# Optimization experiments

Measured on AMD Instinct MI355X. Metric: run time of the kernel, lower is better.

The kernel has to match this reference:

```python
import jax, jax.numpy as jnp
import numpy as np

B, S, D = 4, 2048, 1024
H = 16
DK = D // H  # 64

def setup_inputs() -> dict:
    key = jax.random.key(0)
    ks = jax.random.split(key, 5)
    scale = 0.02
    return {
        "x": jax.random.normal(ks[0], (B, S, D), dtype=jnp.float32),
        "Wq": jax.random.normal(ks[1], (D, D), dtype=jnp.float32) * scale,
        "Wk": jax.random.normal(ks[2], (D, D), dtype=jnp.float32) * scale,
        "Wv": jax.random.normal(ks[3], (D, D), dtype=jnp.float32) * scale,
        "Wo": jax.random.normal(ks[4], (D, D), dtype=jnp.float32) * scale,
    }

def reference(x, Wq, Wk, Wv, Wo):
    b, s, d = x.shape
    h, dk = H, DK
    # torch nn.Linear(bias=False): y = x @ W.T
    q = (x @ Wq.T).reshape(b, s, h, dk).transpose(0, 2, 1, 3)  # [b,h,s,dk]
    k = (x @ Wk.T).reshape(b, s, h, dk).transpose(0, 2, 1, 3)
    v = (x @ Wv.T).reshape(b, s, h, dk).transpose(0, 2, 1, 3)
    scores = jnp.einsum('bhqd,bhkd->bhqk', q, k) * (dk ** -0.5)
    causal = jnp.triu(jnp.ones((s, s), dtype=bool), k=1)  # True = masked out
    scores = jnp.where(causal, -jnp.inf, scores)
    probs = jax.nn.softmax(scores, axis=-1)
    attn = jnp.einsum('bhqk,bhkd->bhqd', probs, v)  # [b,h,s,dk]
    attn = attn.transpose(0, 2, 1, 3).reshape(b, s, d)
    return attn @ Wo.T
```

## Files before the change

### kernel.cpp

```cpp
#include <hip/hip_runtime.h>

typedef __attribute__((ext_vector_type(8))) short bf16x8;
typedef __attribute__((ext_vector_type(4))) float f32x4;
typedef __attribute__((ext_vector_type(2))) unsigned int u32x2;
typedef unsigned int u32;
typedef unsigned short u16;

constexpr int Bb = 4, S = 2048, D = 1024, H = 16, DK = 64, M = Bb * S;

#if __has_builtin(__builtin_amdgcn_exp2f)
#define EXP2F __builtin_amdgcn_exp2f
#else
#define EXP2F exp2f
#endif

__device__ __forceinline__ u16 f2bf(float f) {
  u32 u = __float_as_uint(f);
  return (u16)((u + 0x7fffu + ((u >> 16) & 1u)) >> 16);
}

__device__ __forceinline__ u32 cvt_pk_bf16(float a, float b) {
  u32 r;
  asm("v_cvt_pk_bf16_f32 %0, %1, %2" : "=v"(r) : "v"(a), "v"(b));
  return r;
}

__device__ __forceinline__ void gld_lds16(const u16* g, u16* l) {
  __builtin_amdgcn_global_load_lds((const __attribute__((address_space(1))) u32*)g,
                                   (__attribute__((address_space(3))) u32*)l, 16, 0, 0);
}

struct CastAll { const float* s[5]; u16* d[5]; float sc[5]; };
__global__ __launch_bounds__(256) void cast_all_kernel(CastAll a) {
  int bid = blockIdx.x;
  int w, off;
  if (bid < 4096) { w = bid >> 10; off = ((bid & 1023) * 256 + threadIdx.x) * 4; }
  else            { w = 4;         off = ((bid - 4096) * 256 + threadIdx.x) * 4; }
  float sc = a.sc[w];
  float4 f = *(const float4*)(a.s[w] + off);
  ushort4 o;
  o.x = f2bf(f.x * sc); o.y = f2bf(f.y * sc); o.z = f2bf(f.z * sc); o.w = f2bf(f.w * sc);
  *(ushort4*)(a.d[w] + off) = o;
}

template <bool OUTF32>
__device__ __forceinline__ void gemm_body(const u16* __restrict__ A,
                                          const u16* __restrict__ Bt,
                                          float* __restrict__ Cf, u16* __restrict__ Cb,
                                          int m0, int n0, u16* As0, u16* As1,
                                          u16* Bs0, u16* Bs1) {
  constexpr int K = 1024;
  const int tid = threadIdx.x, wave = tid >> 6, lane = tid & 63;
  const int quad = lane >> 4, col = lane & 15;
  const int wm = wave >> 1, wn = wave & 1;

  const u16* pA[4];
  u16* dA0[4]; u16* dA1[4];
#pragma unroll
  for (int j = 0; j < 4; j++) {
    int gl = tid + j * 512;
    int r = gl >> 3, sl = gl & 7;
    int kof = (sl ^ (r & 7)) * 8;
    pA[j] = A + (size_t)(m0 + r) * K + kof;
    dA0[j] = As0 + gl * 8; dA1[j] = As1 + gl * 8;
  }
  const u16* pB[2];
  u16* dB0[2]; u16* dB1[2];
#pragma unroll
  for (int j = 0; j < 2; j++) {
    int gl = tid + j * 512;
    int r = gl >> 3, sl = gl & 7;
    int kof = (sl ^ (r & 7)) * 8;
    pB[j] = Bt + (size_t)(n0 + r) * K + kof;
    dB0[j] = Bs0 + gl * 8; dB1[j] = Bs1 + gl * 8;
  }
  const u16* rdA0[4]; const u16* rdA1[4];
  const u16* rdB0[4]; const u16* rdB1[4];
#pragma unroll
  for (int mi = 0; mi < 4; mi++) {
    int R = wm * 64 + mi * 16 + col;
    rdA0[mi] = As0 + R * 64 + ((quad ^ (R & 7)) << 3);
    rdA1[mi] = As1 + R * 64 + ((quad ^ (R & 7)) << 3);
  }
#pragma unroll
  for (int ni = 0; ni < 4; ni++) {
    int R = wn * 64 + ni * 16 + col;
    rdB0[ni] = Bs0 + R * 64 + ((quad ^ (R & 7)) << 3);
    rdB1[ni] = Bs1 + R * 64 + ((quad ^ (R & 7)) << 3);
  }
  int dkbA[4], dkbB[4];
#pragma unroll
  for (int mi = 0; mi < 4; mi++) {
    int R = wm * 64 + mi * 16 + col;
    dkbA[mi] = ((((4 + quad) ^ (R & 7)) - (quad ^ (R & 7))) << 3);
  }
#pragma unroll
  for (int ni = 0; ni < 4; ni++) {
    int R = wn * 64 + ni * 16 + col;
    dkbB[ni] = ((((4 + quad) ^ (R & 7)) - (quad ^ (R & 7))) << 3);
  }

  f32x4 acc[4][4];
#pragma unroll
  for (int i = 0; i < 4; i++)
#pragma unroll
    for (int j = 0; j < 4; j++) acc[i][j] = (f32x4){0.f, 0.f, 0.f, 0.f};

  auto stage = [&](u16* const* dA, u16* const* dB) {
#pragma unroll
    for (int j = 0; j < 4; j++) gld_lds16(pA[j], dA[j]);
#pragma unroll
    for (int j = 0; j < 2; j++) gld_lds16(pB[j], dB[j]);
#pragma unroll
    for (int j = 0; j < 4; j++) pA[j] += 64;
#pragma unroll
    for (int j = 0; j < 2; j++) pB[j] += 64;
  };

  auto compute = [&](const u16* const* rdA, const u16* const* rdB) {
    bf16x8 af[4][2], bfr[4][2];
#pragma unroll
    for (int mi = 0; mi < 4; mi++) {
      af[mi][0] = *(const bf16x8*)(rdA[mi]);
      af[mi][1] = *(const bf16x8*)(rdA[mi] + dkbA[mi]);
    }
#pragma unroll
    for (int ni = 0; ni < 4; ni++) {
      bfr[ni][0] = *(const bf16x8*)(rdB[ni]);
      bfr[ni][1] = *(const bf16x8*)(rdB[ni] + dkbB[ni]);
    }
#pragma unroll
    for (int kb = 0; kb < 2; kb++)
#pragma unroll
      for (int mi = 0; mi < 4; mi++)
#pragma unroll
        for (int ni = 0; ni < 4; ni++)
          acc[mi][ni] = __builtin_amdgcn_mfma_f32_16x16x32_bf16(af[mi][kb], bfr[ni][kb], acc[mi][ni], 0, 0, 0);
  };

  stage(dA0, dB0);

#pragma unroll 1
  for (int t2 = 0; t2 < 8; t2++) {
    __builtin_amdgcn_sched_barrier(0);
    __builtin_amdgcn_s_barrier();
    __builtin_amdgcn_sched_barrier(0);
    stage(dA1, dB1);
    asm volatile("s_waitcnt vmcnt(6)" ::: "memory");
    __builtin_amdgcn_sched_barrier(0);
    __builtin_amdgcn_s_barrier();
    __builtin_amdgcn_sched_barrier(0);
    compute(rdA0, rdB0);
    __builtin_amdgcn_sched_barrier(0);
    __builtin_amdgcn_s_barrier();
    __builtin_amdgcn_sched_barrier(0);
    if (t2 < 7) {
      stage(dA0, dB0);
      asm volatile("s_waitcnt vmcnt(6)" ::: "memory");
    } else {
      asm volatile("s_waitcnt vmcnt(0)" ::: "memory");
    }
    __builtin_amdgcn_sched_barrier(0);
    __builtin_amdgcn_s_barrier();
    __builtin_amdgcn_sched_barrier(0);
    compute(rdA1, rdB1);
  }

#pragma unroll
  for (int mi = 0; mi < 4; mi++)
#pragma unroll
    for (int ni = 0; ni < 4; ni++)
#pragma unroll
      for (int r = 0; r < 4; r++) {
        int row = m0 + wm * 64 + mi * 16 + quad * 4 + r;
        int cc = n0 + wn * 64 + ni * 16 + col;
        float v = acc[mi][ni][r];
        if (OUTF32) Cf[(size_t)row * D + cc] = v;
        else Cb[(size_t)row * D + cc] = f2bf(v);
      }
}

struct QkvArgs { const u16* bt[3]; u16* c[3]; };
__global__ __launch_bounds__(512) void gemm_qkv(const u16* __restrict__ A, QkvArgs q) {
  __shared__ __align__(16) u16 As[2][256 * 64];
  __shared__ __align__(16) u16 Bs[2][128 * 64];
  int sel = blockIdx.x >> 3;
  int n0 = (blockIdx.x & 7) * 128, m0 = blockIdx.y * 256;
  gemm_body<false>(A, q.bt[sel], nullptr, q.c[sel], m0, n0, As[0], As[1], Bs[0], Bs[1]);
}

__global__ __launch_bounds__(512) void gemm_f32(const u16* __restrict__ A,
                                                const u16* __restrict__ Bt,
                                                float* __restrict__ C) {
  __shared__ __align__(16) u16 As[2][256 * 64];
  __shared__ __align__(16) u16 Bs[2][128 * 64];
  gemm_body<true>(A, Bt, C, nullptr, blockIdx.y * 256, blockIdx.x * 128, As[0], As[1], Bs[0], Bs[1]);
}

__global__ __launch_bounds__(256) void attn_kernel(const u16* __restrict__ Q,
                                                   const u16* __restrict__ K,
                                                   const u16* __restrict__ V,
                                                   u16* __restrict__ O) {
  __shared__ __align__(16) u16 Ks[2][2][64 * 32];
  __shared__ __align__(16) u16 Vt[2][64 * 64];
  __shared__ __align__(16) u16 Pw[4][32 * 64];
  const int tid = threadIdx.x, wave = tid >> 6, lane = tid & 63;
  const int quad = lane >> 4, col = lane & 15;
  const int bh = blockIdx.x, b = bh >> 4, h = bh & 15;
  const int pair = blockIdx.y;
  const size_t base = (size_t)b * S * D + h * DK;

  const int vk0 = (tid & 31) * 2;
  const int vdg = tid >> 5;

  bf16x8 bones;
#pragma unroll
  for (int e = 0; e < 8; e++) bones[e] = (short)0x3F80;

  const int rsw = col & 7;
  const int ksl = ((quad ^ ((col >> 1) & 3)) & 3) << 3;
  const u16* kbase[2] = { &Ks[0][0][col * 32 + ksl], &Ks[1][0][col * 32 + ksl] };
  const int vsl0 = ((quad ^ rsw) & 7) << 3;
  const int vsl1 = (((4 + quad) ^ rsw) & 7) << 3;
  const u16* vbase[2] = { &Vt[0][col * 64], &Vt[1][col * 64] };
  u16* pww[2] = { &Pw[wave][col * 64 + (quad & 1) * 4],
                  &Pw[wave][(16 + col) * 64 + (quad & 1) * 4] };
  int swof[4];
#pragma unroll
  for (int n16 = 0; n16 < 4; n16++)
    swof[n16] = (((n16 * 2 + (quad >> 1)) ^ rsw) & 7) << 3;
  const u16* apbase[2] = { &Pw[wave][col * 64], &Pw[wave][(16 + col) * 64] };
  const int kk = tid >> 2;
  const int dch = (tid & 3) ^ ((kk >> 1) & 3);
  const int cb = wave * 64;
  u16* dk[2][2] = { { &Ks[0][0][cb * 8], &Ks[0][1][cb * 8] },
                    { &Ks[1][0][cb * 8], &Ks[1][1][cb * 8] } };
  const int kgrp = vk0 >> 3, kin = vk0 & 7;
  u16* vwb[2] = { &Vt[0][vdg * 8 * 64 + kin], &Vt[1][vdg * 8 * 64 + kin] };
  int vwof[8];
#pragma unroll
  for (int e = 0; e < 8; e++) vwof[e] = e * 64 + ((kgrp ^ e) & 7) * 8;

  auto vstage = [&](const int buf, bf16x8 r0, bf16x8 r1) {
    u16* wb = vwb[buf];
#pragma unroll
    for (int e = 0; e < 8; e++) {
      u32 val = ((u32)(u16)r0[e]) | ((u32)(u16)r1[e] << 16);
      *(u32*)(wb + vwof[e]) = val;
    }
  };

  for (int half = 0; half < 2; half++) {
    const int qb = half ? pair : 15 - pair;
    const int qw = qb * 128 + wave * 32;
    const int nkt = 2 * qb + 2;

    bf16x8 aq[2][2];
#pragma unroll
    for (int mi = 0; mi < 2; mi++)
#pragma unroll
      for (int kb = 0; kb < 2; kb++)
        aq[mi][kb] = *(const bf16x8*)(Q + base + (size_t)(qw + mi * 16 + col) * D + kb * 32 + quad * 8);

    f32x4 ao[2][4], lacc[2];
#pragma unroll
    for (int mi = 0; mi < 2; mi++) {
      lacc[mi] = (f32x4){0.f, 0.f, 0.f, 0.f};
#pragma unroll
      for (int dg = 0; dg < 4; dg++) ao[mi][dg] = (f32x4){0.f, 0.f, 0.f, 0.f};
    }

    auto compute = [&](const int BF, int kt) {
      const u16* kbK = kbase[BF];
      bf16x8 bk0[4], bk1[4];
#pragma unroll
      for (int n16 = 0; n16 < 4; n16++) {
        bk0[n16] = *(const bf16x8*)(kbK + n16 * 512);
        bk1[n16] = *(const bf16x8*)(kbK + n16 * 512 + 2048);
      }
      f32x4 sacc[2][4];
#pragma unroll
      for (int qi = 0; qi < 2; qi++)
#pragma unroll
        for (int n16 = 0; n16 < 4; n16++) sacc[qi][n16] = (f32x4){0.f, 0.f, 0.f, 0.f};
      __builtin_amdgcn_s_setprio(1);
#pragma unroll
      for (int qi = 0; qi < 2; qi++)
#pragma unroll
        for (int n16 = 0; n16 < 4; n16++) {
          sacc[qi][n16] = __builtin_amdgcn_mfma_f32_16x16x32_bf16(bk0[n16], aq[qi][0], sacc[qi][n16], 0, 0, 0);
          sacc[qi][n16] = __builtin_amdgcn_mfma_f32_16x16x32_bf16(bk1[n16], aq[qi][1], sacc[qi][n16], 0, 0, 0);
        }
      __builtin_amdgcn_s_setprio(0);
      const bool full = (kt * 64 + 63) <= qw;
#pragma unroll
      for (int qi = 0; qi < 2; qi++) {
        const int qg = qw + qi * 16 + col;
#pragma unroll
        for (int n16 = 0; n16 < 4; n16++) {
          float p0 = EXP2F(sacc[qi][n16][0]);
          float p1 = EXP2F(sacc[qi][n16][1]);
          float p2 = EXP2F(sacc[qi][n16][2]);
          float p3 = EXP2F(sacc[qi][n16][3]);
          if (!full) {
            int kg = kt * 64 + n16 * 16 + quad * 4;
            p0 = (kg + 0 > qg) ? 0.f : p0;
            p1 = (kg + 1 > qg) ? 0.f : p1;
            p2 = (kg + 2 > qg) ? 0.f : p2;
            p3 = (kg + 3 > qg) ? 0.f : p3;
          }
          u32 lo = cvt_pk_bf16(p0, p1);
          u32 hi = cvt_pk_bf16(p2, p3);
          *(u32x2*)(pww[qi] + swof[n16]) = (u32x2){lo, hi};
        }
      }
      const u16* vtB = vbase[BF];
      bf16x8 bv0[4], bv1[4];
#pragma unroll
      for (int dg = 0; dg < 4; dg++) {
        bv0[dg] = *(const bf16x8*)(vtB + dg * 1024 + vsl0);
        bv1[dg] = *(const bf16x8*)(vtB + dg * 1024 + vsl1);
      }
#pragma unroll
      for (int mi = 0; mi < 2; mi++) {
        bf16x8 ap0 = *(const bf16x8*)(apbase[mi] + vsl0);
        bf16x8 ap1 = *(const bf16x8*)(apbase[mi] + vsl1);
        __builtin_amdgcn_s_setprio(1);
#pragma unroll
        for (int dg = 0; dg < 4; dg++) {
          ao[mi][dg] = __builtin_amdgcn_mfma_f32_16x16x32_bf16(ap0, bv0[dg], ao[mi][dg], 0, 0, 0);
          ao[mi][dg] = __builtin_amdgcn_mfma_f32_16x16x32_bf16(ap1, bv1[dg], ao[mi][dg], 0, 0, 0);
        }
        lacc[mi] = __builtin_amdgcn_mfma_f32_16x16x32_bf16(ap0, bones, lacc[mi], 0, 0, 0);
        lacc[mi] = __builtin_amdgcn_mfma_f32_16x16x32_bf16(ap1, bones, lacc[mi], 0, 0, 0);
        __builtin_amdgcn_s_setprio(0);
      }
    };

    bf16x8 vA0, vA1, vB0, vB1;
    const u16* gv = V + base + (size_t)vk0 * D + vdg * 8;
    vA0 = *(const bf16x8*)gv;
    vA1 = *(const bf16x8*)(gv + D);
    __syncthreads();
    const u16* gk = K + base + (size_t)kk * D + dch * 8;
    gld_lds16(gk, dk[0][0]);
    gld_lds16(gk + 32, dk[0][1]);
    gk += (size_t)64 * D;
    vstage(0, vA0, vA1);
    vB0 = *(const bf16x8*)(gv + (size_t)64 * D);
    vB1 = *(const bf16x8*)(gv + (size_t)64 * D + D);
    gv += (size_t)128 * D;

    for (int kt = 0; kt < nkt; kt += 2) {
      __syncthreads();
      {
        gld_lds16(gk, dk[1][0]);
        gld_lds16(gk + 32, dk[1][1]);
        gk += (size_t)64 * D;
        vstage(1, vB0, vB1);
        if (kt + 2 < nkt) {
          vA0 = *(const bf16x8*)gv;
          vA1 = *(const bf16x8*)(gv + D);
          gv += (size_t)64 * D;
        }
        if (kt * 64 <= qw + 31) compute(0, kt);
      }
      __syncthreads();
      {
        const int kt1 = kt + 1;
        if (kt1 + 1 < nkt) {
          gld_lds16(gk, dk[0][0]);
          gld_lds16(gk + 32, dk[0][1]);
          gk += (size_t)64 * D;
          vstage(0, vA0, vA1);
          if (kt1 + 2 < nkt) {
            vB0 = *(const bf16x8*)gv;
            vB1 = *(const bf16x8*)(gv + D);
            gv += (size_t)64 * D;
          }
        }
        if (kt1 * 64 <= qw + 31) compute(1, kt1);
      }
    }
#pragma unroll
    for (int mi = 0; mi < 2; mi++)
#pragma unroll
      for (int r = 0; r < 4; r++) {
        float inv = 1.f / lacc[mi][r];
        int q = qw + mi * 16 + quad * 4 + r;
#pragma unroll
        for (int dg = 0; dg < 4; dg++)
          O[base + (size_t)q * D + dg * 16 + col] = f2bf(ao[mi][dg][r] * inv);
      }
  }
}

extern "C" void kernel_launch(void* const* d_in, const int* in_sizes, int n_in,
                              void* d_out, int out_size, void* d_ws, size_t ws_size,
                              hipStream_t stream) {
  const float* x  = (const float*)d_in[0];
  const float* Wq = (const float*)d_in[1];
  const float* Wk = (const float*)d_in[2];
  const float* Wv = (const float*)d_in[3];
  const float* Wo = (const float*)d_in[4];

  u16* xb  = (u16*)d_ws;
  u16* wqb = xb + (size_t)M * D;
  u16* wkb = wqb + (size_t)D * D;
  u16* wvb = wkb + (size_t)D * D;
  u16* wob = wvb + (size_t)D * D;
  u16* Qb  = wob + (size_t)D * D;
  u16* Kb  = Qb + (size_t)M * D;
  u16* Vb  = Kb + (size_t)M * D;
  u16* Ab  = xb;

  CastAll ca;
  ca.s[0] = Wq; ca.s[1] = Wk; ca.s[2] = Wv; ca.s[3] = Wo; ca.s[4] = x;
  ca.d[0] = wqb; ca.d[1] = wkb; ca.d[2] = wvb; ca.d[3] = wob; ca.d[4] = xb;
  ca.sc[0] = 0.18033688011112042f;
  ca.sc[1] = 1.f; ca.sc[2] = 1.f; ca.sc[3] = 1.f; ca.sc[4] = 1.f;
  cast_all_kernel<<<4096 + M * D / 1024, 256, 0, stream>>>(ca);

  QkvArgs qa;
  qa.bt[0] = wqb; qa.bt[1] = wkb; qa.bt[2] = wvb;
  qa.c[0] = Qb; qa.c[1] = Kb; qa.c[2] = Vb;
  gemm_qkv<<<dim3(24, M / 256), 512, 0, stream>>>(xb, qa);

  attn_kernel<<<dim3(Bb * H, 8), 256, 0, stream>>>(Qb, Kb, Vb, Ab);

  gemm_f32<<<dim3(D / 128, M / 256), 512, 0, stream>>>(Ab, wob, (float*)d_out);
}
```

Before: 248.6 us.

## Triple-buffer GEMM LDS staging with one barrier per k-step

Replaces the double-buffered GEMM main loop with a three-stage LDS ring, prefetching two k-tiles ahead and using a single barrier per iteration instead of two. The aim is to hide more global-load latency and cut synchronization overhead in the QKV and output projections. LDS per block grows from 96KB to 144KB, and the loop is now fully unrolled, which raises code size and may affect register allocation.

New measurement: 249.6 us. No clear change (+0.4%).

```diff
diff --git a/kernel.cpp b/kernel.cpp
--- a/kernel.cpp
+++ b/kernel.cpp
@@ -47,57 +47,53 @@
 __device__ __forceinline__ void gemm_body(const u16* __restrict__ A,
                                           const u16* __restrict__ Bt,
                                           float* __restrict__ Cf, u16* __restrict__ Cb,
-                                          int m0, int n0, u16* As0, u16* As1,
-                                          u16* Bs0, u16* Bs1) {
+                                          int m0, int n0, u16* AsB, u16* BsB) {
   constexpr int K = 1024;
+  constexpr int ASZ = 256 * 64, BSZ = 128 * 64;
   const int tid = threadIdx.x, wave = tid >> 6, lane = tid & 63;
   const int quad = lane >> 4, col = lane & 15;
   const int wm = wave >> 1, wn = wave & 1;
 
   const u16* pA[4];
-  u16* dA0[4]; u16* dA1[4];
+  u16* dA[3][4];
 #pragma unroll
   for (int j = 0; j < 4; j++) {
     int gl = tid + j * 512;
     int r = gl >> 3, sl = gl & 7;
     int kof = (sl ^ (r & 7)) * 8;
     pA[j] = A + (size_t)(m0 + r) * K + kof;
-    dA0[j] = As0 + gl * 8; dA1[j] = As1 + gl * 8;
+#pragma unroll
+    for (int bi = 0; bi < 3; bi++) dA[bi][j] = AsB + bi * ASZ + gl * 8;
   }
   const u16* pB[2];
-  u16* dB0[2]; u16* dB1[2];
+  u16* dB[3][2];
 #pragma unroll
   for (int j = 0; j < 2; j++) {
     int gl = tid + j * 512;
     int r = gl >> 3, sl = gl & 7;
     int kof = (sl ^ (r & 7)) * 8;
     pB[j] = Bt + (size_t)(n0 + r) * K + kof;
-    dB0[j] = Bs0 + gl * 8; dB1[j] = Bs1 + gl * 8;
-  }
-  const u16* rdA0[4]; const u16* rdA1[4];
-  const u16* rdB0[4]; const u16* rdB1[4];
+#pragma unroll
+    for (int bi = 0; bi < 3; bi++) dB[bi][j] = BsB + bi * BSZ + gl * 8;
+  }
+  const u16* rdA[3][4];
+  const u16* rdB[3][4];
+  int dkbA[4], dkbB[4];
 #pragma unroll
   for (int mi = 0; mi < 4; mi++) {
     int R = wm * 64 + mi * 16 + col;
-    rdA0[mi] = As0 + R * 64 + ((quad ^ (R & 7)) << 3);
-    rdA1[mi] = As1 + R * 64 + ((quad ^ (R & 7)) << 3);
+    int c0 = (quad ^ (R & 7)) << 3;
+    dkbA[mi] = ((((4 + quad) ^ (R & 7)) << 3) - c0);
+#pragma unroll
+    for (int bi = 0; bi < 3; bi++) rdA[bi][mi] = AsB + bi * ASZ + R * 64 + c0;
   }
 #pragma unroll
   for (int ni = 0; ni < 4; ni++) {
     int R = wn * 64 + ni * 16 + col;
-    rdB0[ni] = Bs0 + R * 64 + ((quad ^ (R & 7)) << 3);
-    rdB1[ni] = Bs1 + R * 64 + ((quad ^ (R & 7)) << 3);
-  }
-  int dkbA[4], dkbB[4];
-#pragma unroll
-  for (int mi = 0; mi < 4; mi++) {
-    int R = wm * 64 + mi * 16 + col;
-    dkbA[mi] = ((((4 + quad) ^ (R & 7)) - (quad ^ (R & 7))) << 3);
-  }
-#pragma unroll
-  for (int ni = 0; ni < 4; ni++) {
-    int R = wn * 64 + ni * 16 + col;
-    dkbB[ni] = ((((4 + quad) ^ (R & 7)) - (quad ^ (R & 7))) << 3);
+    int c0 = (quad ^ (R & 7)) << 3;
+    dkbB[ni] = ((((4 + quad) ^ (R & 7)) << 3) - c0);
+#pragma unroll
+    for (int bi = 0; bi < 3; bi++) rdB[bi][ni] = BsB + bi * BSZ + R * 64 + c0;
   }
 
   f32x4 acc[4][4];
@@ -106,28 +102,24 @@
 #pragma unroll
     for (int j = 0; j < 4; j++) acc[i][j] = (f32x4){0.f, 0.f, 0.f, 0.f};
 
-  auto stage = [&](u16* const* dA, u16* const* dB) {
-#pragma unroll
-    for (int j = 0; j < 4; j++) gld_lds16(pA[j], dA[j]);
-#pragma unroll
-    for (int j = 0; j < 2; j++) gld_lds16(pB[j], dB[j]);
-#pragma unroll
-    for (int j = 0; j < 4; j++) pA[j] += 64;
-#pragma unroll
-    for (int j = 0; j < 2; j++) pB[j] += 64;
+  auto stage = [&](int bi) {
+#pragma unroll
+    for (int j = 0; j < 4; j++) { gld_lds16(pA[j], dA[bi][j]); pA[j] += 64; }
+#pragma unroll
+    for (int j = 0; j < 2; j++) { gld_lds16(pB[j], dB[bi][j]); pB[j] += 64; }
   };
 
-  auto compute = [&](const u16* const* rdA, const u16* const* rdB) {
+  auto compute = [&](int bi) {
     bf16x8 af[4][2], bfr[4][2];
 #pragma unroll
     for (int mi = 0; mi < 4; mi++) {
-      af[mi][0] = *(const bf16x8*)(rdA[mi]);
-      af[mi][1] = *(const bf16x8*)(rdA[mi] + dkbA[mi]);
+      af[mi][0] = *(const bf16x8*)(rdA[bi][mi]);
+      af[mi][1] = *(const bf16x8*)(rdA[bi][mi] + dkbA[mi]);
     }
 #pragma unroll
     for (int ni = 0; ni < 4; ni++) {
-      bfr[ni][0] = *(const bf16x8*)(rdB[ni]);
-      bfr[ni][1] = *(const bf16x8*)(rdB[ni] + dkbB[ni]);
+      bfr[ni][0] = *(const bf16x8*)(rdB[bi][ni]);
+      bfr[ni][1] = *(const bf16x8*)(rdB[bi][ni] + dkbB[ni]);
     }
 #pragma unroll
     for (int kb = 0; kb < 2; kb++)
@@ -138,32 +130,18 @@
           acc[mi][ni] = __builtin_amdgcn_mfma_f32_16x16x32_bf16(af[mi][kb], bfr[ni][kb], acc[mi][ni], 0, 0, 0);
   };
 
-  stage(dA0, dB0);
-
-#pragma unroll 1
-  for (int t2 = 0; t2 < 8; t2++) {
+  stage(0);
+  stage(1);
+
+#pragma unroll
+  for (int t = 0; t < 16; t++) {
+    if (t == 15) asm volatile("s_waitcnt vmcnt(0)" ::: "memory");
+    else         asm volatile("s_waitcnt vmcnt(6)" ::: "memory");
     __builtin_amdgcn_sched_barrier(0);
     __builtin_amdgcn_s_barrier();
     __builtin_amdgcn_sched_barrier(0);
-    stage(dA1, dB1);
-    asm volatile("s_waitcnt vmcnt(6)" ::: "memory");
-    __builtin_amdgcn_sched_barrier(0);
-    __builtin_amdgcn_s_barrier();
-    __builtin_amdgcn_sched_barrier(0);
-    compute(rdA0, rdB0);
-    __builtin_amdgcn_sched_barrier(0);
-    __builtin_amdgcn_s_barrier();
-    __builtin_amdgcn_sched_barrier(0);
-    if (t2 < 7) {
-      stage(dA0, dB0);
-      asm volatile("s_waitcnt vmcnt(6)" ::: "memory");
-    } else {
-      asm volatile("s_waitcnt vmcnt(0)" ::: "memory");
-    }
-    __builtin_amdgcn_sched_barrier(0);
-    __builtin_amdgcn_s_barrier();
-    __builtin_amdgcn_sched_barrier(0);
-    compute(rdA1, rdB1);
+    if (t + 2 < 16) stage((t + 2) % 3);
+    compute(t % 3);
   }
 
 #pragma unroll
@@ -182,19 +160,19 @@
 
 struct QkvArgs { const u16* bt[3]; u16* c[3]; };
 __global__ __launch_bounds__(512) void gemm_qkv(const u16* __restrict__ A, QkvArgs q) {
-  __shared__ __align__(16) u16 As[2][256 * 64];
-  __shared__ __align__(16) u16 Bs[2][128 * 64];
+  __shared__ __align__(16) u16 As[3][256 * 64];
+  __shared__ __align__(16) u16 Bs[3][128 * 64];
   int sel = blockIdx.x >> 3;
   int n0 = (blockIdx.x & 7) * 128, m0 = blockIdx.y * 256;
-  gemm_body<false>(A, q.bt[sel], nullptr, q.c[sel], m0, n0, As[0], As[1], Bs[0], Bs[1]);
+  gemm_body<false>(A, q.bt[sel], nullptr, q.c[sel], m0, n0, As[0], Bs[0]);
 }
 
 __global__ __launch_bounds__(512) void gemm_f32(const u16* __restrict__ A,
                                                 const u16* __restrict__ Bt,
                                                 float* __restrict__ C) {
-  __shared__ __align__(16) u16 As[2][256 * 64];
-  __shared__ __align__(16) u16 Bs[2][128 * 64];
-  gemm_body<true>(A, Bt, C, nullptr, blockIdx.y * 256, blockIdx.x * 128, As[0], As[1], Bs[0], Bs[1]);
+  __shared__ __align__(16) u16 As[3][256 * 64];
+  __shared__ __align__(16) u16 Bs[3][128 * 64];
+  gemm_body<true>(A, Bt, C, nullptr, blockIdx.y * 256, blockIdx.x * 128, As[0], Bs[0]);
 }
 
 __global__ __launch_bounds__(256) void attn_kernel(const u16* __restrict__ Q,
```
